# Kernel optimization log

Measured on AMD Instinct MI355X. Metric: run time of the kernel, lower is better.

## Reference

```python
import jax, jax.numpy as jnp
import numpy as np

CODEBOOK_DIM = 8
CODEBOOK_SIZE = 8192
INPUT_DIM = 1024
B, T = 8, 2048


def setup_inputs() -> dict:
    key = jax.random.key(0)
    ks = jax.random.split(key, 6)
    z = jax.random.normal(ks[0], (B, INPUT_DIM, T), dtype=jnp.float32)
    # weight_norm(Conv1d(k=1)) is a reparameterization; effective weight is a dense matrix
    W_in = jax.random.normal(ks[1], (CODEBOOK_DIM, INPUT_DIM), dtype=jnp.float32) * 0.03
    b_in = jax.random.normal(ks[2], (CODEBOOK_DIM,), dtype=jnp.float32) * 0.01
    W_out = jax.random.normal(ks[3], (INPUT_DIM, CODEBOOK_DIM), dtype=jnp.float32) * 0.1
    b_out = jax.random.normal(ks[4], (INPUT_DIM,), dtype=jnp.float32) * 0.01
    codebook = jax.random.normal(ks[5], (CODEBOOK_SIZE, CODEBOOK_DIM), dtype=jnp.float32)
    return {"z": z, "W_in": W_in, "b_in": b_in, "W_out": W_out, "b_out": b_out,
            "codebook": codebook}


def _l2norm(x, axis=-1, eps=1e-12):
    # matches torch F.normalize: x / max(||x||, eps)
    n = jnp.sqrt(jnp.sum(x * x, axis=axis, keepdims=True))
    return x / jnp.maximum(n, eps)


def reference(z, W_in, b_in, W_out, b_out, codebook):
    # in-project: 1x1 conv == matmul over channel dim. z_e: [B, 8, T]
    z_e = jnp.einsum('dc,bct->bdt', W_in, z) + b_in[None, :, None]

    # decode latents: flatten to [B*T, 8], normalize both sides
    enc = z_e.transpose(0, 2, 1).reshape(-1, CODEBOOK_DIM)
    enc_n = _l2norm(enc)
    cb_n = _l2norm(codebook)
    dist = (jnp.sum(enc_n * enc_n, axis=1, keepdims=True)
            - 2.0 * enc_n @ cb_n.T
            + jnp.sum(cb_n * cb_n, axis=1)[None, :])  # [B*T, 8192]
    indices = jnp.argmax(-dist, axis=1).reshape(B, T)  # [B, T]

    # gather UNnormalized codebook vectors, back to [B, 8, T]
    z_q = codebook[indices].transpose(0, 2, 1)

    # straight-through estimator
    z_q = z_e + jax.lax.stop_gradient(z_q - z_e)

    # out-project
    out = jnp.einsum('cd,bdt->bct', W_out, z_q) + b_out[None, :, None]
    return out, indices, z_e
```

## Files before the change

kernel.cpp:

```cpp
#include <hip/hip_runtime.h>
#include <hip/hip_bf16.h>
#include <float.h>

#define B_   8
#define T_   2048
#define CIN  1024
#define DD   8
#define KC   8192
#define NTOK (B_*T_)
#define NSLICE 16
#define SLICE (KC/NSLICE)

#define IDX_OFF ((size_t)B_*CIN*T_)
#define ZE_OFF  (IDX_OFF + NTOK)

#define WS_ENCN  0
#define WS_SE    (WS_ENCN + NTOK*DD)
#define WS_PDIST (WS_SE + NTOK)
#define WS_PIDX  (WS_PDIST + NSLICE*NTOK)

__global__ __launch_bounds__(256) void inproj(const float* __restrict__ z,
                                              const float* __restrict__ W_in,
                                              const float* __restrict__ b_in,
                                              float* __restrict__ out,
                                              float* __restrict__ ws) {
    __shared__ float wt[CIN * DD];
    __shared__ float red[8][32][DD];
    int tid = threadIdx.x;
    for (int idx = tid; idx < CIN * DD; idx += 256) {
        int d = idx >> 10, c = idx & 1023;
        wt[c * 8 + d] = W_in[idx];
    }
    __syncthreads();

    int bid = blockIdx.x;
    int b  = bid >> 6;
    int tg = bid & 63;
    int t0 = tg * 32;
    int g = tid >> 5, tl = tid & 31;

    const float* zp = z + ((size_t)b * CIN) * T_ + (t0 + tl);
    float acc[8] = {0, 0, 0, 0, 0, 0, 0, 0};
    int cbeg = g * 128;
    #pragma unroll 8
    for (int c = cbeg; c < cbeg + 128; ++c) {
        float v = zp[(size_t)c * T_];
        const float4* w4 = (const float4*)&wt[c * DD];
        float4 w0 = w4[0], w1 = w4[1];
        acc[0] = fmaf(w0.x, v, acc[0]);
        acc[1] = fmaf(w0.y, v, acc[1]);
        acc[2] = fmaf(w0.z, v, acc[2]);
        acc[3] = fmaf(w0.w, v, acc[3]);
        acc[4] = fmaf(w1.x, v, acc[4]);
        acc[5] = fmaf(w1.y, v, acc[5]);
        acc[6] = fmaf(w1.z, v, acc[6]);
        acc[7] = fmaf(w1.w, v, acc[7]);
    }
    #pragma unroll
    for (int d = 0; d < 8; ++d) red[g][tl][d] = acc[d];
    __syncthreads();

    if (tid < 32) {
        int tt = tid;
        float ze[8];
        #pragma unroll
        for (int d = 0; d < 8; ++d) {
            float s01 = (red[0][tt][d] + red[1][tt][d]) + (red[2][tt][d] + red[3][tt][d]);
            float s23 = (red[4][tt][d] + red[5][tt][d]) + (red[6][tt][d] + red[7][tt][d]);
            ze[d] = (s01 + s23) + b_in[d];
        }
        float* zeo = out + ZE_OFF + ((size_t)b * DD) * T_ + (t0 + tt);
        #pragma unroll
        for (int d = 0; d < 8; ++d) zeo[(size_t)d * T_] = ze[d];
        float s2 = __fmul_rn(ze[0], ze[0]);
        #pragma unroll
        for (int d = 1; d < 8; ++d) s2 = __fadd_rn(s2, __fmul_rn(ze[d], ze[d]));
        float m = fmaxf(sqrtf(s2), 1e-12f);
        float en[8];
        #pragma unroll
        for (int d = 0; d < 8; ++d) en[d] = ze[d] / m;
        float se = __fmul_rn(en[0], en[0]);
        #pragma unroll
        for (int d = 1; d < 8; ++d) se = __fadd_rn(se, __fmul_rn(en[d], en[d]));
        int token = b * T_ + t0 + tt;
        float4* ep = (float4*)(ws + WS_ENCN + (size_t)token * DD);
        ep[0] = make_float4(en[0], en[1], en[2], en[3]);
        ep[1] = make_float4(en[4], en[5], en[6], en[7]);
        ws[WS_SE + token] = se;
    }
}

__global__ __launch_bounds__(256) void vq_search(const float* __restrict__ cb,
                                                 float* __restrict__ ws) {
    __shared__ float lcb[SLICE * DD];
    __shared__ float lsc[SLICE];
    int tid = threadIdx.x;
    int bid = blockIdx.x;
    int sl = bid & (NSLICE - 1);
    int tg = bid >> 4;

    #pragma unroll
    for (int r = 0; r < 2; ++r) {
        int jl = tid + r * 256;
        const float4* src = (const float4*)(cb + (size_t)(sl * SLICE + jl) * DD);
        float4 a = src[0], bv = src[1];
        float c[8] = {a.x, a.y, a.z, a.w, bv.x, bv.y, bv.z, bv.w};
        float s2 = __fmul_rn(c[0], c[0]);
        #pragma unroll
        for (int k = 1; k < 8; ++k) s2 = __fadd_rn(s2, __fmul_rn(c[k], c[k]));
        float m = fmaxf(sqrtf(s2), 1e-12f);
        float cn[8];
        #pragma unroll
        for (int k = 0; k < 8; ++k) cn[k] = c[k] / m;
        float sc = __fmul_rn(cn[0], cn[0]);
        #pragma unroll
        for (int k = 1; k < 8; ++k) sc = __fadd_rn(sc, __fmul_rn(cn[k], cn[k]));
        float4* dst = (float4*)&lcb[jl * DD];
        dst[0] = make_float4(cn[0], cn[1], cn[2], cn[3]);
        dst[1] = make_float4(cn[4], cn[5], cn[6], cn[7]);
        lsc[jl] = sc;
    }
    __syncthreads();

    int token = tg * 256 + tid;
    const float4* ep4 = (const float4*)(ws + WS_ENCN + (size_t)token * DD);
    float4 ea = ep4[0], eb = ep4[1];
    float se = ws[WS_SE + token];

    float best = FLT_MAX;
    int bi = 0;
    #pragma unroll 8
    for (int j = 0; j < SLICE; ++j) {
        const float4* c4 = (const float4*)&lcb[j * DD];
        float4 ca = c4[0], cbv = c4[1];
        float dot = ea.x * ca.x;
        dot = fmaf(ea.y, ca.y, dot);
        dot = fmaf(ea.z, ca.z, dot);
        dot = fmaf(ea.w, ca.w, dot);
        dot = fmaf(eb.x, cbv.x, dot);
        dot = fmaf(eb.y, cbv.y, dot);
        dot = fmaf(eb.z, cbv.z, dot);
        dot = fmaf(eb.w, cbv.w, dot);
        float dist = __fadd_rn(fmaf(-2.f, dot, se), lsc[j]);
        bool p = dist < best;
        best = p ? dist : best;
        bi   = p ? j : bi;
    }
    ws[WS_PDIST + (size_t)sl * NTOK + token] = best;
    ((int*)ws)[WS_PIDX + (size_t)sl * NTOK + token] = sl * SLICE + bi;
}

__global__ __launch_bounds__(256) void outproj(const float* __restrict__ ws,
                                               const float* __restrict__ cb,
                                               const float* __restrict__ W_out,
                                               const float* __restrict__ b_out,
                                               float* __restrict__ out) {
    __shared__ float zq[DD * 64];
    int tid = threadIdx.x;
    int bid = blockIdx.x;
    int b   = bid >> 6;
    int rem = bid & 63;
    int tg  = rem >> 1;
    int cg  = rem & 1;
    int t0 = tg * 64;

    if (tid < 64) {
        int tl = tid;
        int token = b * T_ + t0 + tl;
        float best = ws[WS_PDIST + token];
        int bi = ((const int*)ws)[WS_PIDX + token];
        #pragma unroll
        for (int s = 1; s < NSLICE; ++s) {
            float d = ws[WS_PDIST + (size_t)s * NTOK + token];
            int i2  = ((const int*)ws)[WS_PIDX + (size_t)s * NTOK + token];
            bool p = d < best;
            best = p ? d : best;
            bi   = p ? i2 : bi;
        }
        out[IDX_OFF + token] = (float)bi;
        const float* zep = out + ZE_OFF + ((size_t)b * DD) * T_ + (t0 + tl);
        const float4* cv4 = (const float4*)(cb + (size_t)bi * DD);
        float4 ca = cv4[0], cbv = cv4[1];
        float cv[8] = {ca.x, ca.y, ca.z, ca.w, cbv.x, cbv.y, cbv.z, cbv.w};
        #pragma unroll
        for (int d = 0; d < 8; ++d) {
            float ze = zep[(size_t)d * T_];
            zq[d * 64 + tl] = __fadd_rn(ze, __fsub_rn(cv[d], ze));
        }
    }
    __syncthreads();

    int cl = tid >> 6, tl = tid & 63;
    float q[8];
    #pragma unroll
    for (int k = 0; k < 8; ++k) q[k] = zq[k * 64 + tl];

    int cbase = cg * 512 + cl * 128;
    float* op = out + ((size_t)b * CIN) * T_ + (t0 + tl);
    #pragma unroll 4
    for (int i = 0; i < 128; ++i) {
        int c = cbase + i;
        const float4* w4 = (const float4*)(W_out + (size_t)c * DD);
        float4 w0 = w4[0], w1 = w4[1];
        float dot = q[0] * w0.x;
        dot = fmaf(q[1], w0.y, dot);
        dot = fmaf(q[2], w0.z, dot);
        dot = fmaf(q[3], w0.w, dot);
        dot = fmaf(q[4], w1.x, dot);
        dot = fmaf(q[5], w1.y, dot);
        dot = fmaf(q[6], w1.z, dot);
        dot = fmaf(q[7], w1.w, dot);
        op[(size_t)c * T_] = dot + b_out[c];
    }
}

extern "C" void kernel_launch(void* const* d_in, const int* in_sizes, int n_in,
                              void* d_out, int out_size, void* d_ws, size_t ws_size,
                              hipStream_t stream) {
    const float* z     = (const float*)d_in[0];
    const float* W_in  = (const float*)d_in[1];
    const float* b_in  = (const float*)d_in[2];
    const float* W_out = (const float*)d_in[3];
    const float* b_out = (const float*)d_in[4];
    const float* cb    = (const float*)d_in[5];
    float* out = (float*)d_out;
    float* ws  = (float*)d_ws;

    inproj<<<NTOK / 32, 256, 0, stream>>>(z, W_in, b_in, out, ws);
    vq_search<<<(NTOK / 256) * NSLICE, 256, 0, stream>>>(cb, ws);
    outproj<<<B_ * 32 * 2, 256, 0, stream>>>(ws, cb, W_out, b_out, out);
}
```

Measured before the change: 194.8 us.

## Register-block VQ search over two tokens and tile outproj with LDS-staged weights

The VQ search kernel now handles two tokens per thread, so each codebook entry read from LDS is reused across two tokens, and the grid is halved. The output projection stages W_out and b_out into skewed shared memory to avoid bank conflicts. Each thread computes four consecutive time steps and writes them with a float4 store, and blocks no longer split the channels. This cuts global weight re-reads and store instruction count but adds a per-block 32KB LDS fill and fewer blocks in the search kernel.

```diff
diff --git a/kernel.cpp b/kernel.cpp
--- a/kernel.cpp
+++ b/kernel.cpp
@@ -1,5 +1,4 @@
 #include <hip/hip_runtime.h>
-#include <hip/hip_bf16.h>
 #include <float.h>
 
 #define B_   8
@@ -18,6 +17,8 @@
 #define WS_SE    (WS_ENCN + NTOK*DD)
 #define WS_PDIST (WS_SE + NTOK)
 #define WS_PIDX  (WS_PDIST + NSLICE*NTOK)
+
+__device__ __forceinline__ int wskew(int c) { return (c << 3) + (((c >> 6) & 7) << 2); }
 
 __global__ __launch_bounds__(256) void inproj(const float* __restrict__ z,
                                               const float* __restrict__ W_in,
@@ -122,32 +123,39 @@
     }
     __syncthreads();
 
-    int token = tg * 256 + tid;
-    const float4* ep4 = (const float4*)(ws + WS_ENCN + (size_t)token * DD);
-    float4 ea = ep4[0], eb = ep4[1];
-    float se = ws[WS_SE + token];
-
-    float best = FLT_MAX;
-    int bi = 0;
-    #pragma unroll 8
+    int token0 = tg * 512 + tid * 2;
+    float e[2][8], se[2];
+    #pragma unroll
+    for (int m = 0; m < 2; ++m) {
+        const float4* ep = (const float4*)(ws + WS_ENCN + (size_t)(token0 + m) * DD);
+        float4 a = ep[0], bv = ep[1];
+        e[m][0] = a.x;  e[m][1] = a.y;  e[m][2] = a.z;  e[m][3] = a.w;
+        e[m][4] = bv.x; e[m][5] = bv.y; e[m][6] = bv.z; e[m][7] = bv.w;
+        se[m] = ws[WS_SE + token0 + m];
+    }
+
+    float best[2] = {FLT_MAX, FLT_MAX};
+    int bi[2] = {0, 0};
+    #pragma unroll 4
     for (int j = 0; j < SLICE; ++j) {
-        const float4* c4 = (const float4*)&lcb[j * DD];
-        float4 ca = c4[0], cbv = c4[1];
-        float dot = ea.x * ca.x;
-        dot = fmaf(ea.y, ca.y, dot);
-        dot = fmaf(ea.z, ca.z, dot);
-        dot = fmaf(ea.w, ca.w, dot);
-        dot = fmaf(eb.x, cbv.x, dot);
-        dot = fmaf(eb.y, cbv.y, dot);
-        dot = fmaf(eb.z, cbv.z, dot);
-        dot = fmaf(eb.w, cbv.w, dot);
-        float dist = __fadd_rn(fmaf(-2.f, dot, se), lsc[j]);
-        bool p = dist < best;
-        best = p ? dist : best;
-        bi   = p ? j : bi;
-    }
-    ws[WS_PDIST + (size_t)sl * NTOK + token] = best;
-    ((int*)ws)[WS_PIDX + (size_t)sl * NTOK + token] = sl * SLICE + bi;
+        float4 ca = *(const float4*)&lcb[j * 8];
+        float4 cbv = *(const float4*)&lcb[j * 8 + 4];
+        float sc = lsc[j];
+        float cd[8] = {ca.x, ca.y, ca.z, ca.w, cbv.x, cbv.y, cbv.z, cbv.w};
+        #pragma unroll
+        for (int m = 0; m < 2; ++m) {
+            float dot = e[m][0] * cd[0];
+            #pragma unroll
+            for (int k = 1; k < 8; ++k) dot = fmaf(e[m][k], cd[k], dot);
+            float dist = __fadd_rn(fmaf(-2.f, dot, se[m]), sc);
+            bool p = dist < best[m];
+            best[m] = p ? dist : best[m];
+            bi[m]   = p ? j : bi[m];
+        }
+    }
+    *(float2*)(ws + WS_PDIST + (size_t)sl * NTOK + token0) = make_float2(best[0], best[1]);
+    *(int2*)((int*)ws + WS_PIDX + (size_t)sl * NTOK + token0) =
+        make_int2(sl * SLICE + bi[0], sl * SLICE + bi[1]);
 }
 
 __global__ __launch_bounds__(256) void outproj(const float* __restrict__ ws,
@@ -155,62 +163,73 @@
                                                const float* __restrict__ W_out,
                                                const float* __restrict__ b_out,
                                                float* __restrict__ out) {
-    __shared__ float zq[DD * 64];
+    __shared__ float wo[8224];
+    __shared__ float bo[1032];
+    __shared__ float zql[DD * 64];
     int tid = threadIdx.x;
+    for (int i = tid; i < CIN * DD; i += 256) {
+        int c = i >> 3, d = i & 7;
+        wo[wskew(c) + d] = W_out[i];
+    }
+    for (int i = tid; i < CIN; i += 256) bo[i + ((i >> 6) & 7)] = b_out[i];
+
     int bid = blockIdx.x;
-    int b   = bid >> 6;
-    int rem = bid & 63;
-    int tg  = rem >> 1;
-    int cg  = rem & 1;
+    int b = bid >> 5, tg = bid & 31;
     int t0 = tg * 64;
 
     if (tid < 64) {
         int tl = tid;
         int token = b * T_ + t0 + tl;
-        float best = ws[WS_PDIST + token];
+        float bestv = ws[WS_PDIST + token];
         int bi = ((const int*)ws)[WS_PIDX + token];
         #pragma unroll
         for (int s = 1; s < NSLICE; ++s) {
             float d = ws[WS_PDIST + (size_t)s * NTOK + token];
             int i2  = ((const int*)ws)[WS_PIDX + (size_t)s * NTOK + token];
-            bool p = d < best;
-            best = p ? d : best;
-            bi   = p ? i2 : bi;
+            bool p = d < bestv;
+            bestv = p ? d : bestv;
+            bi    = p ? i2 : bi;
         }
         out[IDX_OFF + token] = (float)bi;
         const float* zep = out + ZE_OFF + ((size_t)b * DD) * T_ + (t0 + tl);
-        const float4* cv4 = (const float4*)(cb + (size_t)bi * DD);
-        float4 ca = cv4[0], cbv = cv4[1];
-        float cv[8] = {ca.x, ca.y, ca.z, ca.w, cbv.x, cbv.y, cbv.z, cbv.w};
+        float4 ca = *(const float4*)(cb + (size_t)bi * DD);
+        float4 cb2 = *(const float4*)(cb + (size_t)bi * DD + 4);
+        float cv[8] = {ca.x, ca.y, ca.z, ca.w, cb2.x, cb2.y, cb2.z, cb2.w};
         #pragma unroll
         for (int d = 0; d < 8; ++d) {
             float ze = zep[(size_t)d * T_];
-            zq[d * 64 + tl] = __fadd_rn(ze, __fsub_rn(cv[d], ze));
-        }
-    }
-    __syncthreads();
-
-    int cl = tid >> 6, tl = tid & 63;
-    float q[8];
-    #pragma unroll
-    for (int k = 0; k < 8; ++k) q[k] = zq[k * 64 + tl];
-
-    int cbase = cg * 512 + cl * 128;
-    float* op = out + ((size_t)b * CIN) * T_ + (t0 + tl);
+            zql[d * 64 + tl] = __fadd_rn(ze, __fsub_rn(cv[d], ze));
+        }
+    }
+    __syncthreads();
+
+    int qi = tid & 15, g = tid >> 4;
+    float q[4][8];
+    #pragma unroll
+    for (int m = 0; m < 4; ++m)
+        #pragma unroll
+        for (int k = 0; k < 8; ++k) q[m][k] = zql[k * 64 + qi * 4 + m];
+
+    float* op = out + ((size_t)b * CIN) * T_ + t0 + qi * 4;
+    int cbeg = g * 64;
+    int bskew = (g & 7);
     #pragma unroll 4
-    for (int i = 0; i < 128; ++i) {
-        int c = cbase + i;
-        const float4* w4 = (const float4*)(W_out + (size_t)c * DD);
-        float4 w0 = w4[0], w1 = w4[1];
-        float dot = q[0] * w0.x;
-        dot = fmaf(q[1], w0.y, dot);
-        dot = fmaf(q[2], w0.z, dot);
-        dot = fmaf(q[3], w0.w, dot);
-        dot = fmaf(q[4], w1.x, dot);
-        dot = fmaf(q[5], w1.y, dot);
-        dot = fmaf(q[6], w1.z, dot);
-        dot = fmaf(q[7], w1.w, dot);
-        op[(size_t)c * T_] = dot + b_out[c];
+    for (int i = 0; i < 64; ++i) {
+        int c = cbeg + i;
+        int w0 = wskew(c);
+        float4 wa = *(const float4*)&wo[w0];
+        float4 wb = *(const float4*)&wo[w0 + 4];
+        float wd[8] = {wa.x, wa.y, wa.z, wa.w, wb.x, wb.y, wb.z, wb.w};
+        float bc = bo[c + bskew];
+        float r[4];
+        #pragma unroll
+        for (int m = 0; m < 4; ++m) {
+            float dot = q[m][0] * wd[0];
+            #pragma unroll
+            for (int k = 1; k < 8; ++k) dot = fmaf(q[m][k], wd[k], dot);
+            r[m] = dot + bc;
+        }
+        *(float4*)(op + (size_t)c * T_) = make_float4(r[0], r[1], r[2], r[3]);
     }
 }
 
@@ -227,6 +246,6 @@
     float* ws  = (float*)d_ws;
 
     inproj<<<NTOK / 32, 256, 0, stream>>>(z, W_in, b_in, out, ws);
-    vq_search<<<(NTOK / 256) * NSLICE, 256, 0, stream>>>(cb, ws);
-    outproj<<<B_ * 32 * 2, 256, 0, stream>>>(ws, cb, W_out, b_out, out);
-}
+    vq_search<<<(NTOK / 512) * NSLICE, 256, 0, stream>>>(cb, ws);
+    outproj<<<NTOK / 64, 256, 0, stream>>>(ws, cb, W_out, b_out, out);
+}
```

Result: no change. 194.0 us (-0.4%).
